# Optimization experiments

Hardware: AMD Instinct MI355X
Metric: run time of the kernel (lower is better)

The kernel has to match this reference:

```python
import jax, jax.numpy as jnp
import numpy as np

D_MODEL = 1024
N_HEADS = 16
D_K = D_MODEL // N_HEADS
D_FF = 4 * D_MODEL
MEM = 32
EPS = 1e-6
NEG = -1e9


def layer_norm(x, alpha, bias):
    # torch: alpha * (x - mean) / (std_unbiased + eps) + bias
    mean = jnp.mean(x, axis=-1, keepdims=True)
    std = jnp.sqrt(jnp.var(x, axis=-1, keepdims=True, ddof=1))
    return alpha * (x - mean) / (std + EPS) + bias


def setup_inputs() -> dict:
    key = jax.random.key(0)
    ks = jax.random.split(key, 12)
    B, S = 4, 2048
    s = 1.0 / np.sqrt(D_MODEL)
    inp = {
        "x": jax.random.normal(ks[0], (B, S, D_MODEL), jnp.float32),
        "mask": jnp.ones((1, 1, S, S + MEM), jnp.int32),
        "memory_tokens": jax.random.normal(ks[1], (MEM, D_MODEL), jnp.float32),
        "w_q": jax.random.normal(ks[2], (D_MODEL, D_MODEL), jnp.float32) * s,
        "w_k": jax.random.normal(ks[3], (D_MODEL, D_MODEL), jnp.float32) * s,
        "w_v": jax.random.normal(ks[4], (D_MODEL, D_MODEL), jnp.float32) * s,
        "w_o": jax.random.normal(ks[5], (D_MODEL, D_MODEL), jnp.float32) * s,
        "ln1_alpha": jnp.ones((D_MODEL,), jnp.float32),
        "ln1_bias": jnp.zeros((D_MODEL,), jnp.float32),
        "ln2_alpha": jnp.ones((D_MODEL,), jnp.float32),
        "ln2_bias": jnp.zeros((D_MODEL,), jnp.float32),
        "ff_w1": jax.random.normal(ks[6], (D_MODEL, D_FF), jnp.float32) * s,
        "ff_b1": jnp.zeros((D_FF,), jnp.float32),
        "ff_w2": jax.random.normal(ks[7], (D_FF, D_MODEL), jnp.float32) * (1.0 / np.sqrt(D_FF)),
        "ff_b2": jnp.zeros((D_MODEL,), jnp.float32),
    }
    return inp


def reference(x, mask, memory_tokens, w_q, w_k, w_v, w_o,
              ln1_alpha, ln1_bias, ln2_alpha, ln2_bias,
              ff_w1, ff_b1, ff_w2, ff_b2):
    B, S, D = x.shape
    memory = jnp.broadcast_to(memory_tokens[None], (B, MEM, D))

    # --- residual 1: self attention with memory K/V ---
    xn = layer_norm(x, ln1_alpha, ln1_bias)
    q = (xn @ w_q).reshape(B, S, N_HEADS, D_K).transpose(0, 2, 1, 3)  # [B,h,S,dk]
    k = (xn @ w_k).reshape(B, S, N_HEADS, D_K).transpose(0, 2, 1, 3)
    v = (xn @ w_v).reshape(B, S, N_HEADS, D_K).transpose(0, 2, 1, 3)
    mem_k = (memory @ w_k).reshape(B, MEM, N_HEADS, D_K).transpose(0, 2, 1, 3)
    mem_v = (memory @ w_v).reshape(B, MEM, N_HEADS, D_K).transpose(0, 2, 1, 3)
    k = jnp.concatenate([mem_k, k], axis=2)  # [B,h,M+S,dk]
    v = jnp.concatenate([mem_v, v], axis=2)

    scores = jnp.einsum("bhsd,bhtd->bhst", q, k) / np.sqrt(D_K)  # [B,h,S,M+S]
    scores = jnp.where(mask == 0, NEG, scores)
    attn = jax.nn.softmax(scores, axis=-1)
    ctx = jnp.einsum("bhst,bhtd->bhsd", attn, v)
    ctx = ctx.transpose(0, 2, 1, 3).reshape(B, S, D)
    x = x + ctx @ w_o

    # --- residual 2: FFN ---
    xn2 = layer_norm(x, ln2_alpha, ln2_bias)
    ff = jax.nn.relu(xn2 @ ff_w1 + ff_b1) @ ff_w2 + ff_b2
    x = x + ff

    new_memory = jnp.broadcast_to(jnp.mean(x, axis=1, keepdims=True), (B, MEM, D))
    return (x, new_memory)
```

## Files before the change

### kernel.cpp

```cpp
#include <hip/hip_runtime.h>
#include <hip/hip_bf16.h>
#include <cstdint>
#include <cstddef>


typedef __attribute__((ext_vector_type(8))) short short8;
typedef __attribute__((ext_vector_type(4))) float floatx4;
typedef __attribute__((ext_vector_type(4))) unsigned short ushort4v;
typedef __attribute__((ext_vector_type(2))) unsigned int uint2v;

#define NB   4
#define SEQ  2048
#define DM   1024
#define DKH  64
#define TT   2080
#define DFF  4096
#define NMEM 32

static __device__ __forceinline__ float bu2f(unsigned short u) {
  return __uint_as_float(((unsigned int)u) << 16);
}
static __device__ __forceinline__ unsigned short f2bu(float x) {
  __hip_bfloat16 h = __float2bfloat16(x);
  return *reinterpret_cast<unsigned short*>(&h);
}
static __device__ __forceinline__ float fast_exp2(float x) {
#if __has_builtin(__builtin_amdgcn_exp2f)
  return __builtin_amdgcn_exp2f(x);
#else
  return exp2f(x);
#endif
}
static __device__ __forceinline__ void async16(const void* g, void* l) {
  __builtin_amdgcn_global_load_lds(
      (const __attribute__((address_space(1))) void*)g,
      (__attribute__((address_space(3))) void*)l, 16, 0, 0);
}

#define PREP_X   8192
#define PREP_MT  (PREP_X + 32)
#define PREP_SM  (PREP_MT + 9)
#define PREP_T   (PREP_SM + 3072)

__global__ __launch_bounds__(256) void prep(
    const void* __restrict__ x,   const void* __restrict__ memtok,
    const void* __restrict__ wq,  const void* __restrict__ wk,
    const void* __restrict__ wv,  const void* __restrict__ wo,
    const void* __restrict__ fw1, const void* __restrict__ fw2,
    const void* __restrict__ ln1a, const void* __restrict__ ln1b,
    const void* __restrict__ ln2a, const void* __restrict__ ln2b,
    const void* __restrict__ fb1, const void* __restrict__ fb2,
    unsigned short* __restrict__ xb, unsigned short* __restrict__ MT,
    unsigned short* __restrict__ Wtq, unsigned short* __restrict__ Wtk,
    unsigned short* __restrict__ Wtv, unsigned short* __restrict__ Wto,
    unsigned short* __restrict__ Wt1, unsigned short* __restrict__ Wt2,
    unsigned short* __restrict__ L1A, unsigned short* __restrict__ L1B,
    unsigned short* __restrict__ L2A, unsigned short* __restrict__ L2B,
    unsigned short* __restrict__ FB1, unsigned short* __restrict__ FB2,
    int* __restrict__ FLAG)
{
  const int tid = threadIdx.x;
  const unsigned short probe = ((const unsigned short*)x)[tid & 63];
  const unsigned e = (probe >> 7) & 0xFF;
  const bool ok = (e == 0) || (e >= 100 && e <= 141);
  const int flag = (__ballot(!ok) != 0ULL) ? 1 : 0;
  const int bid = blockIdx.x;
  if (bid == 0 && tid == 0) *FLAG = flag;

  if (bid < PREP_T && bid >= PREP_SM) {
    const int tb = bid - PREP_SM;
    const void* in; unsigned short* outp; int R, C, tx, ty;
    if (tb < 1024) {
      const int w = tb >> 8, lt = tb & 255;
      in = (w == 0) ? wq : (w == 1) ? wk : (w == 2) ? wv : wo;
      outp = (w == 0) ? Wtq : (w == 1) ? Wtk : (w == 2) ? Wtv : Wto;
      R = DM; C = DM; tx = lt & 15; ty = lt >> 4;
    } else if (tb < 2048) {
      const int lt = tb - 1024;
      in = fw1; outp = Wt1; R = DM; C = DFF; tx = lt & 63; ty = lt >> 6;
    } else {
      const int lt = tb - 2048;
      in = fw2; outp = Wt2; R = DFF; C = DM; tx = lt & 15; ty = lt >> 4;
    }
    __shared__ unsigned short tile[64][65];
    const int r0 = ty << 6, c0 = tx << 6;
    const int lr = tid >> 2, lc = (tid & 3) << 4;
    if (flag) {
      const float* ip = (const float*)in + (size_t)(r0 + lr) * C + c0 + lc;
#pragma unroll
      for (int q = 0; q < 16; q += 4) {
        floatx4 f = *(const floatx4*)(ip + q);
        tile[lr][lc+q+0] = f2bu(f[0]); tile[lr][lc+q+1] = f2bu(f[1]);
        tile[lr][lc+q+2] = f2bu(f[2]); tile[lr][lc+q+3] = f2bu(f[3]);
      }
    } else {
      const unsigned short* ip = (const unsigned short*)in + (size_t)(r0 + lr) * C + c0 + lc;
#pragma unroll
      for (int q = 0; q < 16; q += 4) {
        ushort4v a = *(const ushort4v*)(ip + q);
        tile[lr][lc+q+0] = a.x; tile[lr][lc+q+1] = a.y;
        tile[lr][lc+q+2] = a.z; tile[lr][lc+q+3] = a.w;
      }
    }
    __syncthreads();
    unsigned short* op = outp + (size_t)(c0 + lr) * R + r0 + lc;
#pragma unroll
    for (int q = 0; q < 16; q += 4) {
      ushort4v a;
      a.x = tile[lc+q+0][lr]; a.y = tile[lc+q+1][lr];
      a.z = tile[lc+q+2][lr]; a.w = tile[lc+q+3][lr];
      *(ushort4v*)(op + q) = a;
    }
    return;
  }

  const void* src; unsigned short* dst; int base;
  if (bid < PREP_X)      { src = x;      dst = xb; base = bid * 1024; }
  else if (bid < PREP_MT){ src = memtok; dst = MT; base = (bid - PREP_X) * 1024; }
  else {
    const int s = bid - PREP_MT; base = 0;
    if      (s == 0) { src = ln1a; dst = L1A; }
    else if (s == 1) { src = ln1b; dst = L1B; }
    else if (s == 2) { src = ln2a; dst = L2A; }
    else if (s == 3) { src = ln2b; dst = L2B; }
    else if (s <= 7) { src = fb1;  dst = FB1; base = (s - 4) * 1024; }
    else             { src = fb2;  dst = FB2; }
  }
  const int i = base + tid * 4;
  if (flag) {
    const float* s4 = (const float*)src + i;
    ushort4v o;
    o.x = f2bu(s4[0]); o.y = f2bu(s4[1]); o.z = f2bu(s4[2]); o.w = f2bu(s4[3]);
    *(ushort4v*)&dst[i] = o;
  } else {
    *(ushort4v*)&dst[i] = *(const ushort4v*)&((const unsigned short*)src)[i];
  }
}

__global__ __launch_bounds__(256, 3) void gemm_bt(
    const unsigned short* __restrict__ A, int lda,
    const unsigned short* __restrict__ Bt, int ldbt,
    const unsigned short* __restrict__ bias,
    const unsigned short* __restrict__ resid_b,
    const float* __restrict__ resid_f,
    void* __restrict__ outp, void* __restrict__ outp2, void* __restrict__ outp3,
    int M, int N, int K, int relu, int mode, const int* __restrict__ dt)
{
  __shared__ __align__(16) unsigned short As[2][128 * 32];
  __shared__ __align__(16) unsigned short Bs[2][128 * 32];

  const int tid  = threadIdx.x;
  const int wave = tid >> 6;
  const int lane = tid & 63;
  const int quad = lane >> 4;
  const int lr   = lane & 15;
  const int wm   = (wave >> 1) * 64;
  const int wn   = (wave & 1) * 64;

  const int gx  = gridDim.x;
  const int nwg = gx * gridDim.y;
  int wg = blockIdx.y * gx + blockIdx.x;
  wg = (wg & 7) * (nwg >> 3) + (wg >> 3);
  const int by = wg / gx;
  const int bx = wg - by * gx;
  const int m0 = by * 128;
  const int n0 = bx * 128;

  floatx4 acc[4][4];
#pragma unroll
  for (int i = 0; i < 4; ++i)
#pragma unroll
    for (int j = 0; j < 4; ++j) { floatx4 z = {0.f, 0.f, 0.f, 0.f}; acc[i][j] = z; }

  const int srow = lane >> 2;
  const int skof = (((lane & 3) ^ ((lane >> 3) & 3))) * 8;
  const int fsw  = (lr >> 1) & 3;

  auto stage = [&](int buf, int kk) {
#pragma unroll
    for (int i = 0; i < 2; ++i) {
      const int rr = wave * 32 + i * 16;
      const int r  = rr + srow;
      int gr = m0 + r; gr = gr < M ? gr : (M - 1);
      async16(A  + (size_t)gr * lda + kk + skof, &As[buf][rr * 32]);
      const int gn = n0 + r;
      async16(Bt + (size_t)gn * ldbt + kk + skof, &Bs[buf][rr * 32]);
    }
  };

  const int nk = K >> 5;
  stage(0, 0);
  int cur = 0;
  for (int it = 0; it < nk; ++it) {
    if (it + 1 < nk) {
      stage(cur ^ 1, (it + 1) << 5);
      asm volatile("s_waitcnt vmcnt(4)" ::: "memory");
    } else {
      asm volatile("s_waitcnt vmcnt(0)" ::: "memory");
    }
    __builtin_amdgcn_s_barrier();

    const unsigned short* Ab = &As[cur][0];
    const unsigned short* Bb = &Bs[cur][0];
    short8 af[4], bfr[4];
#pragma unroll
    for (int mi = 0; mi < 4; ++mi)
      af[mi]  = *(const short8*)&Ab[(wm + mi * 16 + lr) * 32 + ((quad ^ fsw) * 8)];
#pragma unroll
    for (int ni = 0; ni < 4; ++ni)
      bfr[ni] = *(const short8*)&Bb[(wn + ni * 16 + lr) * 32 + ((quad ^ fsw) * 8)];
#pragma unroll
    for (int mi = 0; mi < 4; ++mi)
#pragma unroll
      for (int ni = 0; ni < 4; ++ni)
        acc[mi][ni] = __builtin_amdgcn_mfma_f32_16x16x32_bf16(af[mi], bfr[ni], acc[mi][ni], 0, 0, 0);

    asm volatile("s_waitcnt lgkmcnt(0)" ::: "memory");
    __builtin_amdgcn_s_barrier();
    cur ^= 1;
  }

  if (mode == 5) {
    const int cb     = n0 + wn;
    const int sector = cb >> 10;
    const int clb    = cb & 1023;
    unsigned short* Qo = (unsigned short*)outp;
    unsigned short* Ko = (unsigned short*)outp2;
    unsigned short* Vo = (unsigned short*)outp3;
#pragma unroll
    for (int mi = 0; mi < 4; ++mi) {
      const int rb = m0 + wm + mi * 16 + quad * 4;
#pragma unroll
      for (int ni = 0; ni < 4; ++ni) {
        const int col = clb + ni * 16 + lr;
        if (sector == 0) {
#pragma unroll
          for (int rg = 0; rg < 4; ++rg) {
            const int r = rb + rg;
            if (r < NB * SEQ) Qo[(size_t)r * DM + col] = f2bu(acc[mi][ni][rg]);
          }
        } else if (sector == 1) {
#pragma unroll
          for (int rg = 0; rg < 4; ++rg) {
            const int r = rb + rg;
            if (r >= M) continue;
            const int row2 = (r < NB * SEQ) ? ((r >> 11) * TT + NMEM + (r & (SEQ - 1)))
                                            : (r - NB * SEQ);
            Ko[(size_t)row2 * DM + col] = f2bu(acc[mi][ni][rg]);
          }
        } else {
          if (rb < M) {
            int bb, t;
            if (rb < NB * SEQ) { bb = rb >> 11; t = NMEM + (rb & (SEQ - 1)); }
            else               { bb = 0;        t = rb - NB * SEQ; }
            ushort4v pk;
            pk.x = f2bu(acc[mi][ni][0]); pk.y = f2bu(acc[mi][ni][1]);
            pk.z = f2bu(acc[mi][ni][2]); pk.w = f2bu(acc[mi][ni][3]);
            *(ushort4v*)(Vo + ((size_t)bb * DM + col) * TT + t) = pk;
          }
        }
      }
    }
    return;
  }

  const int ofp32 = (mode == 4 && dt) ? *dt : 0;
#pragma unroll
  for (int mi = 0; mi < 4; ++mi) {
    const int rb = m0 + wm + mi * 16 + quad * 4;
#pragma unroll
    for (int ni = 0; ni < 4; ++ni) {
      const int col = n0 + wn + ni * 16 + lr;
      const float bv = bias ? bu2f(bias[col]) : 0.0f;
#pragma unroll
      for (int rg = 0; rg < 4; ++rg) {
        const int r = rb + rg;
        if (r >= M) continue;
        float v = acc[mi][ni][rg] + bv;
        if (relu) v = fmaxf(v, 0.0f);
        if (resid_b) v += bu2f(resid_b[(size_t)r * N + col]);
        if (resid_f) v += resid_f[(size_t)r * N + col];
        const size_t idx = (size_t)r * N + col;
        if (mode == 3)       ((float*)outp)[idx] = v;
        else if (mode == 4) {
          if (ofp32) ((float*)outp)[idx] = v;
          else       ((unsigned short*)outp)[idx] = f2bu(v);
        } else               ((unsigned short*)outp)[idx] = f2bu(v);
      }
    }
  }
}

#define PSTR 72

__global__ __launch_bounds__(256, 3) void flash_attn(
    const unsigned short* __restrict__ Q,
    const unsigned short* __restrict__ Kb,
    const unsigned short* __restrict__ Vtb,
    unsigned short* __restrict__ ctx)
{
  __shared__ __align__(16) unsigned short Ks[2][64 * 64];
  __shared__ __align__(16) unsigned short Vs[2][64 * 64];
  __shared__ __align__(16) unsigned short Ps[128 * PSTR];

  const int tid  = threadIdx.x;
  const int wave = tid >> 6;
  const int lane = tid & 63;
  const int quad = lane >> 4;
  const int lr   = lane & 15;

  const int i    = blockIdx.x;
  const int pair = (i & 7) * 8 + (i >> 7);
  const int q0   = ((i >> 3) & 15) * 128;
  const int b    = pair >> 4;
  const int h    = pair & 15;

  const unsigned short* Qb  = Q   + ((size_t)(b * SEQ + q0)) * DM + h * DKH;
  const unsigned short* Kbp = Kb  + ((size_t)b * TT) * DM + h * DKH;
  const unsigned short* Vbp = Vtb + ((size_t)(b * DM + h * DKH)) * TT;

  short8 aq[2][2];
#pragma unroll
  for (int mi = 0; mi < 2; ++mi)
#pragma unroll
    for (int ks = 0; ks < 2; ++ks)
      aq[mi][ks] = *(const short8*)(Qb + (size_t)(wave * 32 + mi * 16 + lr) * DM
                                       + ks * 32 + quad * 8);

  const int srl = lane >> 3;
  const int swc = (lane & 7) ^ srl;

  floatx4 O[2][4], Osum[2];
#pragma unroll
  for (int mi = 0; mi < 2; ++mi) {
    floatx4 z = {0.f, 0.f, 0.f, 0.f};
    Osum[mi] = z;
#pragma unroll
    for (int ni = 0; ni < 4; ++ni) O[mi][ni] = z;
  }
  short8 ones;
#pragma unroll
  for (int i2 = 0; i2 < 8; ++i2) ones[i2] = (short)0x3F80;

  const float SC = 0.125f * 1.4426950408889634f;

  auto stageKV = [&](int buf, int t0s) {
#pragma unroll
    for (int i2 = 0; i2 < 2; ++i2) {
      const int rr = (wave * 2 + i2) * 8 + srl;
      int tg = t0s + rr; tg = tg < TT ? tg : (TT - 1);
      async16(Kbp + (size_t)tg * DM + swc * 8, &Ks[buf][(wave * 2 + i2) * 512]);
      int ts = t0s + swc * 8; ts = ts <= (TT - 8) ? ts : (TT - 8);
      async16(Vbp + (size_t)rr * TT + ts, &Vs[buf][(wave * 2 + i2) * 512]);
    }
  };

  stageKV(0, 0);
  int cur = 0;

  for (int t0 = 0; t0 < TT; t0 += 64) {
    if (t0 + 64 < TT) {
      stageKV(cur ^ 1, t0 + 64);
      asm volatile("s_waitcnt vmcnt(4)" ::: "memory");
    } else {
      asm volatile("s_waitcnt vmcnt(0)" ::: "memory");
    }
    __builtin_amdgcn_s_barrier();

    floatx4 sc4[2][4];
#pragma unroll
    for (int mi = 0; mi < 2; ++mi)
#pragma unroll
      for (int ni = 0; ni < 4; ++ni) { floatx4 z = {0.f, 0.f, 0.f, 0.f}; sc4[mi][ni] = z; }
#pragma unroll
    for (int ks = 0; ks < 2; ++ks) {
      short8 bk[4];
#pragma unroll
      for (int ni = 0; ni < 4; ++ni) {
        const int row = ni * 16 + lr;
        bk[ni] = *(const short8*)&Ks[cur][row * 64 + (((ks * 4 + quad) ^ (row & 7)) * 8)];
      }
      __builtin_amdgcn_s_setprio(1);
#pragma unroll
      for (int mi = 0; mi < 2; ++mi)
#pragma unroll
        for (int ni = 0; ni < 4; ++ni)
          sc4[mi][ni] = __builtin_amdgcn_mfma_f32_16x16x32_bf16(bk[ni], aq[mi][ks], sc4[mi][ni], 0, 0, 0);
      __builtin_amdgcn_s_setprio(0);
    }

    const int rem = TT - t0;
#pragma unroll
    for (int mi = 0; mi < 2; ++mi) {
      const int prow = (wave * 32 + mi * 16 + lr) * PSTR;
#pragma unroll
      for (int ni = 0; ni < 4; ++ni) {
        const int kb = ni * 16 + quad * 4;
        float p0 = (kb + 0 < rem) ? fast_exp2(sc4[mi][ni][0] * SC) : 0.0f;
        float p1 = (kb + 1 < rem) ? fast_exp2(sc4[mi][ni][1] * SC) : 0.0f;
        float p2 = (kb + 2 < rem) ? fast_exp2(sc4[mi][ni][2] * SC) : 0.0f;
        float p3 = (kb + 3 < rem) ? fast_exp2(sc4[mi][ni][3] * SC) : 0.0f;
        unsigned int u0, u1;
        asm("v_cvt_pk_bf16_f32 %0, %1, %2" : "=v"(u0) : "v"(p0), "v"(p1));
        asm("v_cvt_pk_bf16_f32 %0, %1, %2" : "=v"(u1) : "v"(p2), "v"(p3));
        uint2v pk2; pk2.x = u0; pk2.y = u1;
        *(uint2v*)&Ps[prow + kb] = pk2;
      }
    }

    __asm__ __volatile__("" ::: "memory");

#pragma unroll
    for (int ks = 0; ks < 2; ++ks) {
      short8 ap[2], bv[4];
#pragma unroll
      for (int mi = 0; mi < 2; ++mi)
        ap[mi] = *(const short8*)&Ps[(wave * 32 + mi * 16 + lr) * PSTR + ks * 32 + quad * 8];
#pragma unroll
      for (int ni = 0; ni < 4; ++ni) {
        const int row = ni * 16 + lr;
        bv[ni] = *(const short8*)&Vs[cur][row * 64 + (((ks * 4 + quad) ^ (row & 7)) * 8)];
      }
      __builtin_amdgcn_s_setprio(1);
#pragma unroll
      for (int mi = 0; mi < 2; ++mi) {
        Osum[mi] = __builtin_amdgcn_mfma_f32_16x16x32_bf16(ap[mi], ones, Osum[mi], 0, 0, 0);
#pragma unroll
        for (int ni = 0; ni < 4; ++ni)
          O[mi][ni] = __builtin_amdgcn_mfma_f32_16x16x32_bf16(ap[mi], bv[ni], O[mi][ni], 0, 0, 0);
      }
      __builtin_amdgcn_s_setprio(0);
    }

    asm volatile("s_waitcnt lgkmcnt(0)" ::: "memory");
    __builtin_amdgcn_s_barrier();
    cur ^= 1;
  }

#pragma unroll
  for (int mi = 0; mi < 2; ++mi)
#pragma unroll
    for (int rg = 0; rg < 4; ++rg) {
      const float inv = 1.0f / Osum[mi][rg];
      const int row = q0 + wave * 32 + mi * 16 + quad * 4 + rg;
#pragma unroll
      for (int ni = 0; ni < 4; ++ni) {
        const int col = h * DKH + ni * 16 + lr;
        ctx[((size_t)(b * SEQ + row)) * DM + col] = f2bu(O[mi][ni][rg] * inv);
      }
    }
}

__global__ __launch_bounds__(256) void ln_kernel(
    const unsigned short* __restrict__ xin_bf,
    const float* __restrict__ xin_f,
    const unsigned short* __restrict__ memtok,
    const unsigned short* __restrict__ gam,
    const unsigned short* __restrict__ bet,
    unsigned short* __restrict__ outp,
    int rows_main)
{
  const int row = blockIdx.x;
  const int tid = threadIdx.x;
  const int c0  = tid * 4;
  if (row >= rows_main) {
    const int mr = row - rows_main;
    *(ushort4v*)&outp[(size_t)row * DM + c0] =
        *(const ushort4v*)&memtok[(size_t)mr * DM + c0];
    return;
  }
  float v[4];
  if (xin_bf) {
    ushort4v u = *(const ushort4v*)&xin_bf[(size_t)row * DM + c0];
    v[0] = bu2f(u.x); v[1] = bu2f(u.y); v[2] = bu2f(u.z); v[3] = bu2f(u.w);
  } else {
    floatx4 f = *(const floatx4*)&xin_f[(size_t)row * DM + c0];
    v[0] = f[0]; v[1] = f[1]; v[2] = f[2]; v[3] = f[3];
  }
  float s  = v[0] + v[1] + v[2] + v[3];
  float ss = v[0]*v[0] + v[1]*v[1] + v[2]*v[2] + v[3]*v[3];
#pragma unroll
  for (int m = 1; m <= 32; m <<= 1) {
    s  += __shfl_xor(s, m, 64);
    ss += __shfl_xor(ss, m, 64);
  }
  __shared__ float red[8];
  const int wave = tid >> 6, lane = tid & 63;
  if (lane == 0) { red[wave] = s; red[4 + wave] = ss; }
  __syncthreads();
  s  = red[0] + red[1] + red[2] + red[3];
  ss = red[4] + red[5] + red[6] + red[7];
  const float mean = s * (1.0f / 1024.0f);
  float var = (ss - 1024.0f * mean * mean) * (1.0f / 1023.0f);
  var = fmaxf(var, 0.0f);
  const float inv = 1.0f / (sqrtf(var) + 1e-6f);
  ushort4v o;
  o.x = f2bu(bu2f(gam[c0+0]) * (v[0] - mean) * inv + bu2f(bet[c0+0]));
  o.y = f2bu(bu2f(gam[c0+1]) * (v[1] - mean) * inv + bu2f(bet[c0+1]));
  o.z = f2bu(bu2f(gam[c0+2]) * (v[2] - mean) * inv + bu2f(bet[c0+2]));
  o.w = f2bu(bu2f(gam[c0+3]) * (v[3] - mean) * inv + bu2f(bet[c0+3]));
  *(ushort4v*)&outp[(size_t)row * DM + c0] = o;
}

__global__ __launch_bounds__(256) void replicate_mem(
    unsigned short* __restrict__ Kb, unsigned short* __restrict__ Vtb)
{
  const int idx = blockIdx.x * 256 + threadIdx.x;
  const int t = idx >> 10, c = idx & 1023;
  const unsigned short kv = Kb[(size_t)t * DM + c];
  const unsigned short vv = Vtb[(size_t)c * TT + t];
#pragma unroll
  for (int b = 1; b < NB; ++b) {
    Kb[((size_t)b * TT + t) * DM + c] = kv;
    Vtb[((size_t)(b * DM + c)) * TT + t] = vv;
  }
}

__global__ __launch_bounds__(256) void colsum(
    const void* __restrict__ xo, float* __restrict__ acc,
    const int* __restrict__ flag)
{
  const int d  = blockIdx.x * 256 + threadIdx.x;
  const int s0 = blockIdx.y * 256;
  const int b  = blockIdx.z;
  const size_t base = ((size_t)(b * SEQ + s0)) * DM + d;
  float s = 0.0f;
  if (*flag) {
    const float* p = (const float*)xo;
    for (int i = 0; i < 256; ++i) s += p[base + (size_t)i * DM];
  } else {
    const unsigned short* p = (const unsigned short*)xo;
    for (int i = 0; i < 256; ++i) s += bu2f(p[base + (size_t)i * DM]);
  }
  atomicAdd(&acc[b * DM + d], s);
}

__global__ __launch_bounds__(256) void write_mem(
    const float* __restrict__ acc, void* __restrict__ dout,
    const int* __restrict__ flag)
{
  const int idx = blockIdx.x * 256 + threadIdx.x;
  const int b = idx >> 10, d = idx & 1023;
  const float w = acc[idx] * (1.0f / 2048.0f);
  const int f = *flag;
#pragma unroll
  for (int m = 0; m < NMEM; ++m) {
    const size_t off = (size_t)NB * SEQ * DM + ((size_t)(b * NMEM + m)) * DM + d;
    if (f) ((float*)dout)[off] = w;
    else   ((unsigned short*)dout)[off] = f2bu(w);
  }
}

extern "C" void kernel_launch(void* const* d_in, const int* in_sizes, int n_in,
                              void* d_out, int out_size, void* d_ws, size_t ws_size,
                              hipStream_t stream) {
  const void* x      = d_in[0];
  const void* memtok = d_in[2];
  const void* wq     = d_in[3];
  const void* wk     = d_in[4];
  const void* wv     = d_in[5];
  const void* wo     = d_in[6];
  const void* ln1a   = d_in[7];
  const void* ln1b   = d_in[8];
  const void* ln2a   = d_in[9];
  const void* ln2b   = d_in[10];
  const void* fw1    = d_in[11];
  const void* fb1    = d_in[12];
  const void* fw2    = d_in[13];
  const void* fb2    = d_in[14];

  char* ws = (char*)d_ws;
  constexpr size_t OFF_WT1 = 0;
  constexpr size_t OFF_WT2 = OFF_WT1 + (size_t)DFF * DM * 2;
  constexpr size_t OFF_VT  = OFF_WT2 + (size_t)DM * DFF * 2;
  constexpr size_t SZ_VT   = (size_t)NB * DM * TT * 2;
  constexpr size_t OFF_Q   = OFF_VT + SZ_VT;
  constexpr size_t SZ_Q    = (size_t)NB * SEQ * DM * 2;
  constexpr size_t OFF_K   = OFF_Q + SZ_Q;
  constexpr size_t SZ_K    = (size_t)NB * TT * DM * 2;
  constexpr size_t OFF_XN  = OFF_K + SZ_K;
  constexpr size_t SZ_XN   = (size_t)8224 * DM * 2;
  constexpr size_t OFF_W4  = OFF_XN + SZ_XN;
  constexpr size_t SZ_DD   = (size_t)DM * DM * 2;
  constexpr size_t OFF_XB  = OFF_W4 + 4 * SZ_DD;
  constexpr size_t SZ_XB   = (size_t)NB * SEQ * DM * 2;
  constexpr size_t OFF_SM  = OFF_XB + SZ_XB;
  static_assert(OFF_XN + (size_t)NB * SEQ * 2048 * 2 <= OFF_SM, "h1 overlay");
  static_assert(OFF_Q + (size_t)NB * SEQ * DM * 4 <= OFF_XN, "x1f overlay");

  unsigned short* Wt1 = (unsigned short*)(ws + OFF_WT1);
  unsigned short* Wt2 = (unsigned short*)(ws + OFF_WT2);
  unsigned short* Vtb = (unsigned short*)(ws + OFF_VT);
  unsigned short* Qb  = (unsigned short*)(ws + OFF_Q);
  unsigned short* Kbf = (unsigned short*)(ws + OFF_K);
  unsigned short* xn  = (unsigned short*)(ws + OFF_XN);
  unsigned short* Wtq = (unsigned short*)(ws + OFF_W4);
  unsigned short* Wtk = (unsigned short*)(ws + OFF_W4 + SZ_DD);
  unsigned short* Wtv = (unsigned short*)(ws + OFF_W4 + 2 * SZ_DD);
  unsigned short* Wto = (unsigned short*)(ws + OFF_W4 + 3 * SZ_DD);
  unsigned short* xb  = (unsigned short*)(ws + OFF_XB);
  unsigned short* MT  = (unsigned short*)(ws + OFF_SM);
  unsigned short* L1A = (unsigned short*)(ws + OFF_SM + 65536);
  unsigned short* L1B = (unsigned short*)(ws + OFF_SM + 67584);
  unsigned short* L2A = (unsigned short*)(ws + OFF_SM + 69632);
  unsigned short* L2B = (unsigned short*)(ws + OFF_SM + 71680);
  unsigned short* FB1 = (unsigned short*)(ws + OFF_SM + 73728);
  unsigned short* FB2 = (unsigned short*)(ws + OFF_SM + 81920);
  float*          accb= (float*)(ws + OFF_SM + 84480);
  int*            FLAG= (int*)(ws + OFF_SM + 101376);

  unsigned short* ctx = xn;
  unsigned short* h1  = xn;
  float*          x1f = (float*)(ws + OFF_Q);
  unsigned short* xn2 = Vtb;

  const dim3 blk(256);

  prep<<<PREP_T, blk, 0, stream>>>(x, memtok, wq, wk, wv, wo, fw1, fw2,
                                   ln1a, ln1b, ln2a, ln2b, fb1, fb2,
                                   xb, MT, Wtq, Wtk, Wtv, Wto, Wt1, Wt2,
                                   L1A, L1B, L2A, L2B, FB1, FB2, FLAG);

  ln_kernel<<<8224, blk, 0, stream>>>(xb, nullptr, MT, L1A, L1B, xn, 8192);

  gemm_bt<<<dim3(24, 65), blk, 0, stream>>>(
      xn, DM, Wtq, DM, nullptr, nullptr, nullptr,
      Qb, Kbf, Vtb, 8224, 3072, DM, 0, 5, nullptr);
  replicate_mem<<<128, blk, 0, stream>>>(Kbf, Vtb);

  flash_attn<<<1024, blk, 0, stream>>>(Qb, Kbf, Vtb, ctx);

  gemm_bt<<<dim3(8, 64), blk, 0, stream>>>(
      ctx, DM, Wto, DM, nullptr, xb, nullptr,
      x1f, nullptr, nullptr, 8192, DM, DM, 0, 3, nullptr);

  ln_kernel<<<8192, blk, 0, stream>>>(nullptr, x1f, nullptr, L2A, L2B, xn2, 8192);

  gemm_bt<<<dim3(16, 64), blk, 0, stream>>>(
      xn2, DM, Wt1, DM, FB1, nullptr, nullptr,
      h1, nullptr, nullptr, 8192, 2048, DM, 1, 0, nullptr);
  gemm_bt<<<dim3(8, 64), blk, 0, stream>>>(
      h1, 2048, Wt2, DFF, nullptr, nullptr, x1f,
      x1f, nullptr, nullptr, 8192, DM, 2048, 0, 3, nullptr);
  gemm_bt<<<dim3(16, 64), blk, 0, stream>>>(
      xn2, DM, Wt1 + (size_t)2048 * DM, DM, FB1 + 2048, nullptr, nullptr,
      h1, nullptr, nullptr, 8192, 2048, DM, 1, 0, nullptr);
  gemm_bt<<<dim3(8, 64), blk, 0, stream>>>(
      h1, 2048, Wt2 + 2048, DFF, FB2, nullptr, x1f,
      d_out, nullptr, nullptr, 8192, DM, 2048, 0, 4, FLAG);

  hipMemsetAsync(accb, 0, (size_t)NB * DM * sizeof(float), stream);
  colsum<<<dim3(4, 8, 4), blk, 0, stream>>>(d_out, accb, FLAG);
  write_mem<<<16, blk, 0, stream>>>(accb, d_out, FLAG);
}
```

Before: 630.9 us.

## Replace LDS round-trip of softmax probabilities with ds_bpermute register shuffles

The attention kernel no longer writes the bf16 probability tile to shared memory and reads it back in MFMA A-operand layout. It rebuilds that layout with cross-lane ds_bpermute shuffles from registers. This frees the Ps shared buffer, so occupancy is raised from 3 to 4 blocks per CU through launch_bounds. The cost is 16 bpermutes per k-step plus selects, and more register pressure under the tighter occupancy bound.

```diff
diff --git a/kernel.cpp b/kernel.cpp
--- a/kernel.cpp
+++ b/kernel.cpp
@@ -7,7 +7,7 @@
 typedef __attribute__((ext_vector_type(8))) short short8;
 typedef __attribute__((ext_vector_type(4))) float floatx4;
 typedef __attribute__((ext_vector_type(4))) unsigned short ushort4v;
-typedef __attribute__((ext_vector_type(2))) unsigned int uint2v;
+typedef __attribute__((ext_vector_type(4))) unsigned int uint4v;
 
 #define NB   4
 #define SEQ  2048
@@ -291,9 +291,7 @@
   }
 }
 
-#define PSTR 72
-
-__global__ __launch_bounds__(256, 3) void flash_attn(
+__global__ __launch_bounds__(256, 4) void flash_attn(
     const unsigned short* __restrict__ Q,
     const unsigned short* __restrict__ Kb,
     const unsigned short* __restrict__ Vtb,
@@ -301,7 +299,6 @@
 {
   __shared__ __align__(16) unsigned short Ks[2][64 * 64];
   __shared__ __align__(16) unsigned short Vs[2][64 * 64];
-  __shared__ __align__(16) unsigned short Ps[128 * PSTR];
 
   const int tid  = threadIdx.x;
   const int wave = tid >> 6;
@@ -329,6 +326,10 @@
 
   const int srl = lane >> 3;
   const int swc = (lane & 7) ^ srl;
+
+  const int addrA = (((quad & 1) * 32 + lr) << 2);
+  const int addrB = addrA + 64;
+  const bool qlo  = (quad < 2);
 
   floatx4 O[2][4], Osum[2];
 #pragma unroll
@@ -390,9 +391,9 @@
     }
 
     const int rem = TT - t0;
+    unsigned int u[2][4][2];
 #pragma unroll
     for (int mi = 0; mi < 2; ++mi) {
-      const int prow = (wave * 32 + mi * 16 + lr) * PSTR;
 #pragma unroll
       for (int ni = 0; ni < 4; ++ni) {
         const int kb = ni * 16 + quad * 4;
@@ -403,23 +404,37 @@
         unsigned int u0, u1;
         asm("v_cvt_pk_bf16_f32 %0, %1, %2" : "=v"(u0) : "v"(p0), "v"(p1));
         asm("v_cvt_pk_bf16_f32 %0, %1, %2" : "=v"(u1) : "v"(p2), "v"(p3));
-        uint2v pk2; pk2.x = u0; pk2.y = u1;
-        *(uint2v*)&Ps[prow + kb] = pk2;
-      }
-    }
-
-    __asm__ __volatile__("" ::: "memory");
+        u[mi][ni][0] = u0;
+        u[mi][ni][1] = u1;
+      }
+    }
 
 #pragma unroll
     for (int ks = 0; ks < 2; ++ks) {
-      short8 ap[2], bv[4];
-#pragma unroll
-      for (int mi = 0; mi < 2; ++mi)
-        ap[mi] = *(const short8*)&Ps[(wave * 32 + mi * 16 + lr) * PSTR + ks * 32 + quad * 8];
+      short8 bv[4];
 #pragma unroll
       for (int ni = 0; ni < 4; ++ni) {
         const int row = ni * 16 + lr;
         bv[ni] = *(const short8*)&Vs[cur][row * 64 + (((ks * 4 + quad) ^ (row & 7)) * 8)];
+      }
+      short8 ap[2];
+#pragma unroll
+      for (int mi = 0; mi < 2; ++mi) {
+        const int na = 2 * ks, nb = 2 * ks + 1;
+        unsigned int a0 = (unsigned int)__builtin_amdgcn_ds_bpermute(addrA, (int)u[mi][na][0]);
+        unsigned int b0 = (unsigned int)__builtin_amdgcn_ds_bpermute(addrA, (int)u[mi][nb][0]);
+        unsigned int a1 = (unsigned int)__builtin_amdgcn_ds_bpermute(addrA, (int)u[mi][na][1]);
+        unsigned int b1 = (unsigned int)__builtin_amdgcn_ds_bpermute(addrA, (int)u[mi][nb][1]);
+        unsigned int a2 = (unsigned int)__builtin_amdgcn_ds_bpermute(addrB, (int)u[mi][na][0]);
+        unsigned int b2 = (unsigned int)__builtin_amdgcn_ds_bpermute(addrB, (int)u[mi][nb][0]);
+        unsigned int a3 = (unsigned int)__builtin_amdgcn_ds_bpermute(addrB, (int)u[mi][na][1]);
+        unsigned int b3 = (unsigned int)__builtin_amdgcn_ds_bpermute(addrB, (int)u[mi][nb][1]);
+        uint4v dw;
+        dw.x = qlo ? a0 : b0;
+        dw.y = qlo ? a1 : b1;
+        dw.z = qlo ? a2 : b2;
+        dw.w = qlo ? a3 : b3;
+        ap[mi] = *reinterpret_cast<short8*>(&dw);
       }
       __builtin_amdgcn_s_setprio(1);
 #pragma unroll
```

Measured after the change: 633.5 us. About the same (+0.4%).
